# Performance work log

Hardware: AMD Instinct MI355X
Metric: run time of the kernel (lower is better)

## Reference

```python
import jax, jax.numpy as jnp
import numpy as np

DELTA = 5.0          # weight on positive BCE term
R = 0.01             # hard-negative fraction
M, N = 4096, 16384   # batch rows, memory-bank size
NUM_HARD = int(R * (N - 1))  # int(r * neg_count); each row has exactly 1 positive


def setup_inputs() -> dict:
    key = jax.random.key(0)
    k1, k2 = jax.random.split(key)
    inputs = jax.random.normal(k1, (M, N), dtype=jnp.float32)
    targets = jax.random.randint(k2, (M,), 0, N)
    return {"inputs": inputs, "targets": targets}


def reference(inputs, targets):
    m, n = inputs.shape
    rows = jnp.arange(m)
    # positive logit per row (one-hot scatter => exactly one positive)
    pos = inputs[rows, targets]                          # [m]
    # BCE with logits, target=1: softplus(-x); mean over the single positive
    l_pos = jax.nn.softplus(-pos)                        # [m]
    # exclude positive from negatives by sinking it to -inf, then hard top-k
    neg_inf = jnp.finfo(inputs.dtype).min
    masked = inputs.at[rows, targets].set(neg_inf)       # [m, n]
    hard_neg, _ = jax.lax.top_k(masked, NUM_HARD)        # [m, NUM_HARD]
    # BCE with logits, target=0: softplus(x); mean over hard negatives
    l_neg = jnp.mean(jax.nn.softplus(hard_neg), axis=1)  # [m]
    return jnp.mean(DELTA * l_pos + l_neg)
```

## Files before the change

### kernel.cpp

```cpp
#include <hip/hip_runtime.h>
#include <stdint.h>

#define M_ROWS 4096
#define N_COLS 16384
#define K_HARD 163
#define DELTA_W 5.0f
#define BLOCK  256
#define SLOTS  12
#define CAP    1024
#define NB     1024
#define SMALL  64
#define THRESH 2.0f
#define KEY_MIN 0xC0000000u

__device__ __forceinline__ uint32_t f2key(float x) {
    uint32_t u = __float_as_uint(x);
    return u ^ (uint32_t)(((int32_t)u >> 31) | 0x80000000u);
}
__device__ __forceinline__ float key2f(uint32_t k) {
    uint32_t u = (k & 0x80000000u) ? (k & 0x7fffffffu) : ~k;
    return __uint_as_float(u);
}
__device__ __forceinline__ float softplus_f(float x) {
    return fmaxf(x, 0.0f) + log1pf(__expf(-fabsf(x)));
}

__device__ void pivot_scan(const uint32_t* hist, int K,
                           int* part, int* pivot, int* krem) {
    const int t = threadIdx.x;
    const int bpt = NB / BLOCK;
    const int base = t * bpt;
    int mypart = 0;
    for (int i = 0; i < bpt; ++i) mypart += (int)hist[base + i];
    part[t] = mypart;
    __syncthreads();
    for (int off = 1; off < BLOCK; off <<= 1) {
        int v = part[t];
        if (t + off < BLOCK) v += part[t + off];
        __syncthreads();
        part[t] = v;
        __syncthreads();
    }
    const int above = part[t] - mypart;
    if (above < K && above + mypart >= K) {
        int running = above;
        for (int b = base + bpt - 1; b >= base; --b) {
            int c = (int)hist[b];
            if (running < K && running + c >= K) { *pivot = b; *krem = K - running; }
            running += c;
        }
    }
    __syncthreads();
}

__global__ __launch_bounds__(BLOCK) void mmcl_kernel(
        const float* __restrict__ inputs,
        const int* __restrict__ targets,
        float* __restrict__ out) {
    __shared__ float    s_slots_f[BLOCK * SLOTS];
    __shared__ uint32_t s_cand[CAP];
    __shared__ int s_wt[4], s_wm[4];
    __shared__ int s_found, s_pivot, s_krem, s_nsmall;
    __shared__ uint32_t s_skey[SMALL];
    __shared__ int s_sidx[SMALL];
    __shared__ float s_fw[4];

    const int row = blockIdx.x;
    const int t = threadIdx.x;
    const int lane = t & 63;
    const int wid = t >> 6;
    const float* rowp = inputs + (size_t)row * N_COLS;
    const int target = targets[row];

    if (t == 0) s_found = -1;

    float* myslots = s_slots_f + t * SLOTS;
    uint32_t cnt = 0;
    const float4* rp4 = (const float4*)rowp;
#pragma unroll 4
    for (int it = 0; it < N_COLS / (BLOCK * 4); ++it) {
        const float4 v = rp4[it * BLOCK + t];
        myslots[min(cnt, (uint32_t)(SLOTS - 1))] = v.x; cnt += (v.x >= THRESH);
        myslots[min(cnt, (uint32_t)(SLOTS - 1))] = v.y; cnt += (v.y >= THRESH);
        myslots[min(cnt, (uint32_t)(SLOTS - 1))] = v.z; cnt += (v.z >= THRESH);
        myslots[min(cnt, (uint32_t)(SLOTS - 1))] = v.w; cnt += (v.w >= THRESH);
    }

    const int stored = (int)min(cnt, (uint32_t)SLOTS);
    int inc = stored;
    for (int off = 1; off < 64; off <<= 1) {
        int y = __shfl_up(inc, off);
        if (lane >= off) inc += y;
    }
    int mx = (int)cnt;
    for (int off = 1; off < 64; off <<= 1)
        mx = max(mx, __shfl_xor(mx, off));
    if (lane == 63) { s_wt[wid] = inc; }
    if (lane == 0)  { s_wm[wid] = mx; }
    __syncthreads();
    const int w0 = s_wt[0], w1 = s_wt[1], w2 = s_wt[2], w3 = s_wt[3];
    const int total = w0 + w1 + w2 + w3;
    const int maxc = max(max(s_wm[0], s_wm[1]), max(s_wm[2], s_wm[3]));
    const int wbase = (wid > 0 ? w0 : 0) + (wid > 1 ? w1 : 0) + (wid > 2 ? w2 : 0);
    const int myoff = wbase + inc - stored;
    for (int c = 0; c < stored; ++c) {
        const int d = myoff + c;
        if (d < CAP) s_cand[d] = f2key(myslots[c]);
    }
    __syncthreads();

    const float pos = rowp[target];
    const uint32_t tkey = f2key(pos);
    const int tclamp = min(total, CAP);
    if (pos >= THRESH) {
        for (int i = t; i < tclamp; i += BLOCK)
            if (s_cand[i] == tkey) { atomicCAS(&s_found, -1, i); break; }
    }
    __syncthreads();
    int ncand = total;
    if (s_found >= 0) {
        ncand = total - 1;
        if (t == 0) s_cand[s_found] = s_cand[ncand];
    }
    __syncthreads();

    const bool fast = (maxc <= SLOTS) && (total <= CAP) && (ncand >= K_HARD);
    bool needfb = !fast;
    float local = 0.0f;

    uint32_t* hist = (uint32_t*)s_slots_f;

    if (fast) {
        for (int i = t; i < NB; i += BLOCK) hist[i] = 0;
        __syncthreads();
        for (int i = t; i < ncand; i += BLOCK)
            atomicAdd(&hist[min((s_cand[i] - KEY_MIN) >> 14, (uint32_t)(NB - 1))], 1u);
        __syncthreads();

        const int base4 = t * 4;
        const int c0 = (int)hist[base4], c1 = (int)hist[base4 + 1],
                  c2 = (int)hist[base4 + 2], c3 = (int)hist[base4 + 3];
        const int own = c0 + c1 + c2 + c3;
        int suf = own;
        for (int off = 1; off < 64; off <<= 1) {
            int y = __shfl_down(suf, off);
            if (lane + off < 64) suf += y;
        }
        if (lane == 0) s_wt[wid] = suf;
        if (t == 0) s_nsmall = 0;
        __syncthreads();
        int wsuf = 0;
        for (int w = wid + 1; w < 4; ++w) wsuf += s_wt[w];
        int run = wsuf + (suf - own);
        {
            const int cs[4] = {c0, c1, c2, c3};
            for (int b = 3; b >= 0; --b) {
                const int c = cs[b];
                if (run < K_HARD && run + c >= K_HARD) {
                    s_pivot = base4 + b; s_krem = K_HARD - run;
                }
                run += c;
            }
        }
        __syncthreads();
        const uint32_t B = (uint32_t)s_pivot;
        const int krem = s_krem;

        for (int i = t; i < ncand; i += BLOCK) {
            const uint32_t k = s_cand[i];
            const uint32_t kb = min((k - KEY_MIN) >> 14, (uint32_t)(NB - 1));
            if (kb > B) local += softplus_f(key2f(k));
            else if (kb == B) {
                const int d = atomicAdd(&s_nsmall, 1);
                if (d < SMALL) { s_skey[d] = k; s_sidx[d] = i; }
            }
        }
        __syncthreads();
        const int m = s_nsmall;
        if (m > SMALL) { needfb = true; local = 0.0f; }
        else {
            for (int i = t; i < m; i += BLOCK) {
                const uint32_t ki = s_skey[i]; const int ii = s_sidx[i];
                int r = 0;
                for (int j = 0; j < m; ++j) {
                    const uint32_t kj = s_skey[j];
                    r += (kj > ki) || (kj == ki && s_sidx[j] < ii);
                }
                if (r < krem) local += softplus_f(key2f(ki));
            }
        }
    }

    if (needfb) {
        local = 0.0f;
        int* part = (int*)s_cand;
        for (int i = t; i < NB; i += BLOCK) hist[i] = 0;
        __syncthreads();
        for (int j = t; j < N_COLS; j += BLOCK) {
            if (j == target) continue;
            atomicAdd(&hist[f2key(rowp[j]) >> 22], 1u);
        }
        __syncthreads();
        pivot_scan(hist, K_HARD, part, &s_pivot, &s_krem);
        const int p1 = s_pivot, k1r = s_krem;

        for (int i = t; i < NB; i += BLOCK) hist[i] = 0;
        __syncthreads();
        for (int j = t; j < N_COLS; j += BLOCK) {
            if (j == target) continue;
            const uint32_t k = f2key(rowp[j]);
            if ((int)(k >> 22) == p1) atomicAdd(&hist[(k >> 12) & 1023u], 1u);
        }
        __syncthreads();
        pivot_scan(hist, k1r, part, &s_pivot, &s_krem);
        const uint32_t pref2 = ((uint32_t)p1 << 10) | (uint32_t)s_pivot;
        const int k2r = s_krem;

        for (int i = t; i < NB; i += BLOCK) hist[i] = 0;
        __syncthreads();
        for (int j = t; j < N_COLS; j += BLOCK) {
            if (j == target) continue;
            const uint32_t k = f2key(rowp[j]);
            if ((k >> 12) == pref2) atomicAdd(&hist[(k >> 2) & 1023u], 1u);
        }
        __syncthreads();
        pivot_scan(hist, k2r, part, &s_pivot, &s_krem);
        const uint32_t pref3 = (pref2 << 10) | (uint32_t)s_pivot;
        const int k3r = s_krem;

        for (int i = t; i < 4; i += BLOCK) hist[i] = 0;
        __syncthreads();
        for (int j = t; j < N_COLS; j += BLOCK) {
            if (j == target) continue;
            const uint32_t k = f2key(rowp[j]);
            if ((k >> 2) == pref3) atomicAdd(&hist[k & 3u], 1u);
        }
        __syncthreads();
        if (t == 0) {
            int running = 0;
            for (int b = 3; b >= 0; --b) {
                const int c = (int)hist[b];
                if (running < k3r && running + c >= k3r) {
                    s_pivot = b; s_krem = k3r - running;
                }
                running += c;
            }
        }
        __syncthreads();
        const uint32_t T = (pref3 << 2) | (uint32_t)s_pivot;
        const int tie = s_krem;

        for (int j = t; j < N_COLS; j += BLOCK) {
            if (j == target) continue;
            const uint32_t k = f2key(rowp[j]);
            if (k > T) local += softplus_f(key2f(k));
        }
        if (t == 0) local += (float)tie * softplus_f(key2f(T));
    }

    for (int off = 32; off > 0; off >>= 1) local += __shfl_down(local, off);
    if (lane == 0) s_fw[wid] = local;
    __syncthreads();
    if (t == 0) {
        const float tot = s_fw[0] + s_fw[1] + s_fw[2] + s_fw[3];
        const float l_neg = tot / (float)K_HARD;
        const float l_pos = softplus_f(-pos);
        const float rowval = (DELTA_W * l_pos + l_neg) * (1.0f / (float)M_ROWS);
        atomicAdd(out, rowval);
    }
}

__global__ void mmcl_zero_out(float* out) { out[0] = 0.0f; }

extern "C" void kernel_launch(void* const* d_in, const int* in_sizes, int n_in,
                              void* d_out, int out_size, void* d_ws, size_t ws_size,
                              hipStream_t stream) {
    const float* inputs = (const float*)d_in[0];
    const int* targets = (const int*)d_in[1];
    float* out = (float*)d_out;
    mmcl_zero_out<<<1, 1, 0, stream>>>(out);
    mmcl_kernel<<<M_ROWS, BLOCK, 0, stream>>>(inputs, targets, out);
}
```

Baseline: 359.7 us.

## Split into a ballot-compacting filter kernel and a selection kernel

The single kernel becomes two. The first streams each row, uses wave ballots to compact float4 groups whose max reaches the threshold into per-wave segments in workspace, and records counts. The second rebuilds per-thread candidate slots from those compact segments, with more slots and a larger candidate capacity, then runs the unchanged histogram selection. This is meant to shorten the per-element slot-writing work in the streaming pass and make it more register and occupancy friendly. In exchange it adds a second launch and a global round trip for the compacted groups.

New measurement: 417.2 us. +16.0%, slower.

```diff
diff --git a/kernel.cpp b/kernel.cpp
--- a/kernel.cpp
+++ b/kernel.cpp
@@ -6,12 +6,13 @@
 #define K_HARD 163
 #define DELTA_W 5.0f
 #define BLOCK  256
-#define SLOTS  12
-#define CAP    1024
+#define THRESH 2.0f
+#define KEY_MIN 0xC0000000u
+#define SEGG   192
+#define CAP    1536
 #define NB     1024
 #define SMALL  64
-#define THRESH 2.0f
-#define KEY_MIN 0xC0000000u
+#define SLOTA  13
 
 __device__ __forceinline__ uint32_t f2key(float x) {
     uint32_t u = __float_as_uint(x);
@@ -53,13 +54,43 @@
     __syncthreads();
 }
 
-__global__ __launch_bounds__(BLOCK) void mmcl_kernel(
+__global__ __launch_bounds__(BLOCK) void k1_filter(
+        const float* __restrict__ inputs,
+        uint32_t* __restrict__ counts,
+        float4* __restrict__ groups) {
+    const int row = blockIdx.x;
+    const int lane = threadIdx.x & 63;
+    const int wid = threadIdx.x >> 6;
+    const float4* rp4 = (const float4*)(inputs + (size_t)row * N_COLS);
+    float4* seg = groups + (size_t)(row * 4 + wid) * SEGG;
+    uint32_t wcount = 0;
+#pragma unroll 4
+    for (int it = 0; it < N_COLS / (BLOCK * 4); ++it) {
+        const float4 v = rp4[wid * 1024 + it * 64 + lane];
+        const float m = fmaxf(fmaxf(v.x, v.y), fmaxf(v.z, v.w));
+        const bool pred = (m >= THRESH);
+        const unsigned long long mask = __ballot(pred);
+        if (pred) {
+            const int below = __builtin_amdgcn_mbcnt_hi(
+                (uint32_t)(mask >> 32),
+                __builtin_amdgcn_mbcnt_lo((uint32_t)mask, 0));
+            const uint32_t off = wcount + (uint32_t)below;
+            if (off < SEGG) seg[off] = v;
+        }
+        wcount += (uint32_t)__popcll(mask);
+    }
+    if (lane == 0) counts[row * 4 + wid] = wcount;
+}
+
+__global__ __launch_bounds__(BLOCK) void k2_select(
         const float* __restrict__ inputs,
         const int* __restrict__ targets,
+        const uint32_t* __restrict__ counts,
+        const float4* __restrict__ groups,
         float* __restrict__ out) {
-    __shared__ float    s_slots_f[BLOCK * SLOTS];
+    __shared__ float    s_slots_f[BLOCK * SLOTA];
     __shared__ uint32_t s_cand[CAP];
-    __shared__ int s_wt[4], s_wm[4];
+    __shared__ int s_wc[4], s_wt[4];
     __shared__ int s_found, s_pivot, s_krem, s_nsmall;
     __shared__ uint32_t s_skey[SMALL];
     __shared__ int s_sidx[SMALL];
@@ -73,39 +104,44 @@
     const int target = targets[row];
 
     if (t == 0) s_found = -1;
-
-    float* myslots = s_slots_f + t * SLOTS;
-    uint32_t cnt = 0;
-    const float4* rp4 = (const float4*)rowp;
-#pragma unroll 4
-    for (int it = 0; it < N_COLS / (BLOCK * 4); ++it) {
-        const float4 v = rp4[it * BLOCK + t];
-        myslots[min(cnt, (uint32_t)(SLOTS - 1))] = v.x; cnt += (v.x >= THRESH);
-        myslots[min(cnt, (uint32_t)(SLOTS - 1))] = v.y; cnt += (v.y >= THRESH);
-        myslots[min(cnt, (uint32_t)(SLOTS - 1))] = v.z; cnt += (v.z >= THRESH);
-        myslots[min(cnt, (uint32_t)(SLOTS - 1))] = v.w; cnt += (v.w >= THRESH);
-    }
-
-    const int stored = (int)min(cnt, (uint32_t)SLOTS);
+    if (t < 4) s_wc[t] = (int)counts[row * 4 + t];
+    __syncthreads();
+    const int cw0 = s_wc[0], cw1 = s_wc[1], cw2 = s_wc[2], cw3 = s_wc[3];
+    const bool ovf = (cw0 > SEGG) | (cw1 > SEGG) | (cw2 > SEGG) | (cw3 > SEGG);
+
+    float* myslots = s_slots_f + t * SLOTA;
+    uint32_t c = 0;
+    if (!ovf) {
+        const int cw = s_wc[wid];
+        const float4* seg = groups + (size_t)(row * 4 + wid) * SEGG;
+#pragma unroll
+        for (int g = 0; g < SEGG / 64; ++g) {
+            const int gi = g * 64 + lane;
+            if (gi < cw) {
+                const float4 v = seg[gi];
+                myslots[min(c, (uint32_t)(SLOTA - 1))] = v.x; c += (v.x >= THRESH);
+                myslots[min(c, (uint32_t)(SLOTA - 1))] = v.y; c += (v.y >= THRESH);
+                myslots[min(c, (uint32_t)(SLOTA - 1))] = v.z; c += (v.z >= THRESH);
+                myslots[min(c, (uint32_t)(SLOTA - 1))] = v.w; c += (v.w >= THRESH);
+            }
+        }
+    }
+
+    const int stored = (int)c;
     int inc = stored;
     for (int off = 1; off < 64; off <<= 1) {
         int y = __shfl_up(inc, off);
         if (lane >= off) inc += y;
     }
-    int mx = (int)cnt;
-    for (int off = 1; off < 64; off <<= 1)
-        mx = max(mx, __shfl_xor(mx, off));
-    if (lane == 63) { s_wt[wid] = inc; }
-    if (lane == 0)  { s_wm[wid] = mx; }
+    if (lane == 63) s_wt[wid] = inc;
     __syncthreads();
     const int w0 = s_wt[0], w1 = s_wt[1], w2 = s_wt[2], w3 = s_wt[3];
     const int total = w0 + w1 + w2 + w3;
-    const int maxc = max(max(s_wm[0], s_wm[1]), max(s_wm[2], s_wm[3]));
     const int wbase = (wid > 0 ? w0 : 0) + (wid > 1 ? w1 : 0) + (wid > 2 ? w2 : 0);
     const int myoff = wbase + inc - stored;
-    for (int c = 0; c < stored; ++c) {
-        const int d = myoff + c;
-        if (d < CAP) s_cand[d] = f2key(myslots[c]);
+    for (int j = 0; j < stored; ++j) {
+        const int d = myoff + j;
+        if (d < CAP) s_cand[d] = f2key(myslots[j]);
     }
     __syncthreads();
 
@@ -124,10 +160,9 @@
     }
     __syncthreads();
 
-    const bool fast = (maxc <= SLOTS) && (total <= CAP) && (ncand >= K_HARD);
+    const bool fast = !ovf && (total <= CAP) && (ncand >= K_HARD);
     bool needfb = !fast;
     float local = 0.0f;
-
     uint32_t* hist = (uint32_t*)s_slots_f;
 
     if (fast) {
@@ -155,11 +190,11 @@
         {
             const int cs[4] = {c0, c1, c2, c3};
             for (int b = 3; b >= 0; --b) {
-                const int c = cs[b];
-                if (run < K_HARD && run + c >= K_HARD) {
+                const int cc = cs[b];
+                if (run < K_HARD && run + cc >= K_HARD) {
                     s_pivot = base4 + b; s_krem = K_HARD - run;
                 }
-                run += c;
+                run += cc;
             }
         }
         __syncthreads();
@@ -239,11 +274,11 @@
         if (t == 0) {
             int running = 0;
             for (int b = 3; b >= 0; --b) {
-                const int c = (int)hist[b];
-                if (running < k3r && running + c >= k3r) {
+                const int cc = (int)hist[b];
+                if (running < k3r && running + cc >= k3r) {
                     s_pivot = b; s_krem = k3r - running;
                 }
-                running += c;
+                running += cc;
             }
         }
         __syncthreads();
@@ -278,6 +313,9 @@
     const float* inputs = (const float*)d_in[0];
     const int* targets = (const int*)d_in[1];
     float* out = (float*)d_out;
+    uint32_t* counts = (uint32_t*)d_ws;
+    float4* groups = (float4*)((char*)d_ws + 65536);
     mmcl_zero_out<<<1, 1, 0, stream>>>(out);
-    mmcl_kernel<<<M_ROWS, BLOCK, 0, stream>>>(inputs, targets, out);
-}
+    k1_filter<<<M_ROWS, BLOCK, 0, stream>>>(inputs, counts, groups);
+    k2_select<<<M_ROWS, BLOCK, 0, stream>>>(inputs, targets, counts, groups, out);
+}
```
